# Performance work log

Measured on AMD Instinct MI355X. Metric: run time of the kernel, lower is better.

The kernel has to match this reference:

```python
import jax, jax.numpy as jnp
import numpy as np
import math

B, C, H, W = 32, 256, 64, 64
AUX, RANK, HID, OS = 64, 64, 256, 8


def _fourier(u):
    # u: [B, r] -> take first r//2, sin/cos with freqs linspace(1, pi)
    half = RANK // 2
    w = jnp.linspace(1.0, math.pi, half, dtype=u.dtype)[None, :]
    u = u[:, :half]
    return jnp.concatenate([jnp.sin(u * w), jnp.cos(u * w)], axis=-1)


def setup_inputs() -> dict:
    key = jax.random.key(0)
    ks = jax.random.split(key, 10)

    def lin(k, fan_in, fan_out):
        k1, k2 = jax.random.split(k)
        Wm = jax.random.normal(k1, (fan_in, fan_out), jnp.float32) * 0.02
        bv = jax.random.normal(k2, (fan_out,), jnp.float32) * 0.02
        return Wm, bv

    d = C + AUX
    W_pre, b_pre = lin(ks[0], d, HID)
    W_bc, b_bc = lin(ks[1], HID, C)
    W_bs, b_bs = lin(ks[2], HID, OS)
    W_pc, b_pc = lin(ks[3], HID, RANK)
    W_ps, b_ps = lin(ks[4], HID, RANK)
    W_Wc, b_Wc = lin(ks[5], HID, C * RANK)
    W_Ws, b_Ws = lin(ks[6], HID, OS * RANK)
    x = jax.random.normal(ks[7], (B, C, H, W), jnp.float32)
    a = jax.random.normal(ks[8], (B, AUX), jnp.float32)
    return dict(x=x, a=a, W_pre=W_pre, b_pre=b_pre, W_bc=W_bc, b_bc=b_bc,
                W_bs=W_bs, b_bs=b_bs, W_pc=W_pc, b_pc=b_pc, W_ps=W_ps,
                b_ps=b_ps, W_Wc=W_Wc, b_Wc=b_Wc, W_Ws=W_Ws, b_Ws=b_Ws)


def _m2dm(x, a, W_pre, b_pre, W_bc, b_bc, W_bs, b_bs, W_pc, b_pc,
          W_ps, b_ps, W_Wc, b_Wc, W_Ws, b_Ws):
    Bn, Cn, Hn, Wn = x.shape
    # DynamicProjection
    g = x.mean(axis=(2, 3))                                    # [B,C] GAP
    h = jax.nn.relu(jnp.concatenate([g, a], axis=-1) @ W_pre + b_pre)
    m_base_c = h @ W_bc + b_bc                                 # [B,C]
    m_base_s = h @ W_bs + b_bs                                 # [B,8]
    phi_c = _fourier(h @ W_pc + b_pc)                          # [B,r]
    phi_s = _fourier(h @ W_ps + b_ps)                          # [B,r]
    Wc = (h @ W_Wc + b_Wc).reshape(Bn, Cn, RANK)
    Ws = (h @ W_Ws + b_Ws).reshape(Bn, OS, RANK)
    c_m = m_base_c * jnp.einsum('bcr,br->bc', Wc, phi_c)
    s_m = m_base_s * jnp.einsum('bsr,br->bs', Ws, phi_s)

    # channel modulation
    xc = x * jax.nn.sigmoid(c_m)[:, :, None, None]

    # SpatialModulation: per-sample cross-shaped 3x3 stencil on [avg,max]
    av = x.mean(axis=1)
    mx = x.max(axis=1)
    y = jnp.stack([av, mx], axis=1)                            # [B,2,H,W]
    p = s_m[:, :8].reshape(Bn, 2, 4)                           # up,down,left,right

    def shift(z, di, dj):
        # s[h,w] = z[h+di, w+dj] with zero padding (matches conv2d padding=1)
        zp = jnp.pad(z, ((0, 0), (0, 0), (1, 1), (1, 1)))
        return zp[:, :, 1 + di:1 + di + Hn, 1 + dj:1 + dj + Wn]

    up = shift(y, -1, 0)   # k[0,1] pairs with input row h-1
    dn = shift(y, 1, 0)    # k[2,1]
    lf = shift(y, 0, -1)   # k[1,0]
    rt = shift(y, 0, 1)    # k[1,2]
    pw = p[..., None, None]                                    # [B,2,4,1,1]
    center = -p.sum(axis=-1)[..., None, None]                  # k[1,1] = -sum
    conv = (pw[:, :, 0] * up + pw[:, :, 1] * dn +
            pw[:, :, 2] * lf + pw[:, :, 3] * rt + center * y).sum(axis=1)  # [B,H,W]
    xs = x * jax.nn.sigmoid(conv)[:, None, :, :]
    return x + xc + xs


def reference(x, a, W_pre, b_pre, W_bc, b_bc, W_bs, b_bs, W_pc, b_pc,
              W_ps, b_ps, W_Wc, b_Wc, W_Ws, b_Ws):
    return _m2dm(x, a, W_pre, b_pre, W_bc, b_bc, W_bs, b_bs, W_pc, b_pc,
                 W_ps, b_ps, W_Wc, b_Wc, W_Ws, b_Ws)
```

## Files before the change

### kernel.cpp

```cpp
#include <hip/hip_runtime.h>
#include <math.h>

#define BN   32
#define CN   256
#define HWN  4096
#define AUXN 64
#define RANKN 64
#define HIDN 256
#define OSN  8

#define WS_GPART 0
#define WS_HT    131072
#define WS_PHIC  139264
#define WS_MBC   141312
#define WS_SM    149504
#define WS_SIGC  149760
#define WS_Y     157952
#define WS_SIGS  420096

__global__ __launch_bounds__(256) void k_stats(const float* __restrict__ x,
                                               float* __restrict__ gpart,
                                               float* __restrict__ y) {
  int b = blockIdx.y, tile = blockIdx.x, t = threadIdx.x;
  int w = t >> 6, l = t & 63;
  __shared__ float csum[256 * 65];
  __shared__ float4 s_comb[4][64];
  __shared__ float4 m_comb[4][64];
  const float4* xb4 = (const float4*)(x + (size_t)b * CN * HWN + tile * 256);
  float4 s4 = {0.f, 0.f, 0.f, 0.f};
  float4 m4 = {-INFINITY, -INFINITY, -INFINITY, -INFINITY};
  int c0 = w << 6;
#pragma unroll 8
  for (int cl = 0; cl < 64; cl++) {
    int c = c0 + cl;
    float4 v = xb4[(size_t)c * 1024 + l];
    s4.x += v.x; s4.y += v.y; s4.z += v.z; s4.w += v.w;
    m4.x = fmaxf(m4.x, v.x); m4.y = fmaxf(m4.y, v.y);
    m4.z = fmaxf(m4.z, v.z); m4.w = fmaxf(m4.w, v.w);
    csum[c * 65 + l] = (v.x + v.y) + (v.z + v.w);
  }
  s_comb[w][l] = s4;
  m_comb[w][l] = m4;
  __syncthreads();
  {
    const volatile float* row = csum + t * 65;
    float g0 = 0.f, g1 = 0.f, g2 = 0.f, g3 = 0.f;
#pragma unroll
    for (int j = 0; j < 64; j += 4) {
      g0 += row[j]; g1 += row[j + 1]; g2 += row[j + 2]; g3 += row[j + 3];
    }
    gpart[(((size_t)b * 16 + tile) << 8) + t] = (g0 + g1) + (g2 + g3);
  }
  if (w == 0) {
    float4 a0 = s_comb[0][l], a1 = s_comb[1][l], a2 = s_comb[2][l], a3 = s_comb[3][l];
    float4 b0 = m_comb[0][l], b1 = m_comb[1][l], b2 = m_comb[2][l], b3 = m_comb[3][l];
    float4 sa, ma;
    sa.x = (a0.x + a1.x) + (a2.x + a3.x);
    sa.y = (a0.y + a1.y) + (a2.y + a3.y);
    sa.z = (a0.z + a1.z) + (a2.z + a3.z);
    sa.w = (a0.w + a1.w) + (a2.w + a3.w);
    ma.x = fmaxf(fmaxf(b0.x, b1.x), fmaxf(b2.x, b3.x));
    ma.y = fmaxf(fmaxf(b0.y, b1.y), fmaxf(b2.y, b3.y));
    ma.z = fmaxf(fmaxf(b0.z, b1.z), fmaxf(b2.z, b3.z));
    ma.w = fmaxf(fmaxf(b0.w, b1.w), fmaxf(b2.w, b3.w));
    const float inv = 1.0f / 256.0f;
    float4 avg = {sa.x * inv, sa.y * inv, sa.z * inv, sa.w * inv};
    ((float4*)(y + (size_t)b * 2 * HWN + tile * 256))[l] = avg;
    ((float4*)(y + ((size_t)b * 2 + 1) * HWN + tile * 256))[l] = ma;
  }
}

__global__ __launch_bounds__(256) void k_head(
    const float* __restrict__ gpart, const float* __restrict__ a,
    const float* __restrict__ W_pre, const float* __restrict__ b_pre,
    const float* __restrict__ W_bc,  const float* __restrict__ b_bc,
    const float* __restrict__ W_bs,  const float* __restrict__ b_bs,
    const float* __restrict__ W_pc,  const float* __restrict__ b_pc,
    const float* __restrict__ W_ps,  const float* __restrict__ b_ps,
    const float* __restrict__ W_Ws,  const float* __restrict__ b_Ws,
    const float* __restrict__ y,
    float* __restrict__ h_t_out, float* __restrict__ phic_out,
    float* __restrict__ mbc_out, float* __restrict__ sigs) {
  int b = blockIdx.x, t = threadIdx.x;
  __shared__ float in_s[320];
  __shared__ float h_s[256];
  __shared__ float phic_s[64], phis_s[64];
  __shared__ float red[512];
  __shared__ float red2[256];
  __shared__ float pc[10];
  {
    float gsum = 0.f;
#pragma unroll
    for (int tile = 0; tile < 16; tile++)
      gsum += gpart[(((size_t)b * 16 + tile) << 8) + t];
    in_s[t] = gsum * (1.0f / 4096.0f);
  }
  if (t < 64) in_s[256 + t] = a[b * 64 + t];
  __syncthreads();
  float acc = b_pre[t];
  for (int k = 0; k < 320; k++) acc = fmaf(in_s[k], W_pre[k * 256 + t], acc);
  float h = fmaxf(acc, 0.f);
  h_s[t] = h;
  h_t_out[t * 32 + b] = h;
  __syncthreads();
  {
    int ui = t & 63, kg = t >> 6, j = ui & 31;
    const float* Wp = (ui < 32) ? W_pc : W_ps;
    float u = 0.f;
    int k0 = kg << 6;
    for (int k = k0; k < k0 + 64; k++) u = fmaf(h_s[k], Wp[k * 64 + j], u);
    red2[(ui << 2) | kg] = u;
  }
  __syncthreads();
  if (t < 64) {
    int j = t & 31;
    const float* bp = (t < 32) ? b_pc : b_ps;
    float u = bp[j] + (red2[t * 4] + red2[t * 4 + 1]) + (red2[t * 4 + 2] + red2[t * 4 + 3]);
    float wj = 1.0f + (float)j * (3.14159265358979323846f - 1.0f) / 31.0f;
    float su = sinf(u * wj), cu = cosf(u * wj);
    float* ph = (t < 32) ? phic_s : phis_s;
    ph[j] = su;
    ph[32 + j] = cu;
  }
  __syncthreads();
  if (t < 64) phic_out[b * 64 + t] = phic_s[t];
  float mb = b_bc[t];
  for (int k = 0; k < 256; k++) mb = fmaf(h_s[k], W_bc[k * 256 + t], mb);
  mbc_out[b * 256 + t] = mb;
#pragma unroll
  for (int i = 0; i < 2; i++) {
    int idx = t + 256 * i;
    int s = idx >> 6, r = idx & 63;
    float v = b_Ws[s * 64 + r];
    for (int k = 0; k < 256; k++) v = fmaf(h_s[k], W_Ws[k * 512 + s * 64 + r], v);
    red[idx] = v * phis_s[r];
  }
  {
    int s = t & 7, kg = t >> 3;
    float v = 0.f;
    int k0 = kg << 3;
#pragma unroll
    for (int k = k0; k < k0 + 8; k++) v = fmaf(h_s[k], W_bs[k * 8 + s], v);
    red2[t] = v;
  }
  __syncthreads();
  if (t < 8) {
    float mbs = b_bs[t];
#pragma unroll
    for (int kg = 0; kg < 32; kg++) mbs += red2[kg * 8 + t];
    float sum = 0.f;
    for (int r = 0; r < 64; r++) sum += red[t * 64 + r];
    pc[t] = mbs * sum;
  }
  __syncthreads();
  if (t == 0) {
    pc[8] = -(pc[0] + pc[1] + pc[2] + pc[3]);
    pc[9] = -(pc[4] + pc[5] + pc[6] + pc[7]);
  }
  __syncthreads();
  const float* yb = y + (size_t)b * 2 * HWN;
  for (int px = t; px < 4096; px += 256) {
    int i = px >> 6, j = px & 63;
    float conv = 0.f;
#pragma unroll
    for (int k = 0; k < 2; k++) {
      const float* yk = yb + k * 4096;
      float up = (i > 0)  ? yk[px - 64] : 0.f;
      float dn = (i < 63) ? yk[px + 64] : 0.f;
      float lf = (j > 0)  ? yk[px - 1]  : 0.f;
      float rt = (j < 63) ? yk[px + 1]  : 0.f;
      conv += pc[k * 4 + 0] * up + pc[k * 4 + 1] * dn + pc[k * 4 + 2] * lf +
              pc[k * 4 + 3] * rt + pc[8 + k] * yk[px];
    }
    sigs[b * 4096 + px] = 1.f / (1.f + expf(-conv));
  }
}

__global__ __launch_bounds__(512) void k_cm(
    const float* __restrict__ W_Wc, const float* __restrict__ b_Wc,
    const float* __restrict__ h_t, const float* __restrict__ phic_ws,
    const float* __restrict__ mbc_ws, float* __restrict__ sigc_out) {
  __shared__ __align__(16) float wsl[16384];
  __shared__ __align__(16) float h_s[8192];
  __shared__ __align__(16) float phi_s[2048];
  __shared__ float red[4096];
  __shared__ float red2[512];
  int t = threadIdx.x, c = blockIdx.x;
  {
    const float4* col4 = (const float4*)(W_Wc + (size_t)c * 64);
    float4* wsl4 = (float4*)wsl;
#pragma unroll
    for (int i4 = t; i4 < 4096; i4 += 512) {
      int k = i4 >> 4, rq = i4 & 15;
      wsl4[i4] = col4[(size_t)k * 4096 + rq];
    }
    const float4* ht4 = (const float4*)h_t;
    float4* hs4 = (float4*)h_s;
#pragma unroll
    for (int i4 = t; i4 < 2048; i4 += 512) hs4[i4] = ht4[i4];
    ((float4*)phi_s)[t] = ((const float4*)phic_ws)[t];
  }
  __syncthreads();
  int rq = t & 15, b8 = (t >> 4) & 3, kg = t >> 6;
  const float4* wv = (const float4*)wsl;
  float4 acc[8];
#pragma unroll
  for (int i = 0; i < 8; i++) acc[i] = {0.f, 0.f, 0.f, 0.f};
#pragma unroll 4
  for (int kk = 0; kk < 32; kk++) {
    int k = (kg << 5) + kk;
    float4 w4 = wv[k * 16 + rq];
    const float4* hp = (const float4*)(h_s + k * 32 + (b8 << 3));
    float4 h0 = hp[0], h1 = hp[1];
    float hv[8] = {h0.x, h0.y, h0.z, h0.w, h1.x, h1.y, h1.z, h1.w};
#pragma unroll
    for (int i = 0; i < 8; i++) {
      acc[i].x = fmaf(hv[i], w4.x, acc[i].x);
      acc[i].y = fmaf(hv[i], w4.y, acc[i].y);
      acc[i].z = fmaf(hv[i], w4.z, acc[i].z);
      acc[i].w = fmaf(hv[i], w4.w, acc[i].w);
    }
  }
  float4 bw = {0.f, 0.f, 0.f, 0.f};
  if (kg == 0) bw = ((const float4*)(b_Wc + (size_t)c * 64))[rq];
#pragma unroll
  for (int i = 0; i < 8; i++) {
    int bb = (b8 << 3) + i;
    float4 ph = ((const float4*)phi_s)[bb * 16 + rq];
    float4 av = acc[i];
    av.x += bw.x; av.y += bw.y; av.z += bw.z; av.w += bw.w;
    red[(kg * 32 + bb) * 16 + rq] =
        (av.x * ph.x + av.y * ph.y) + (av.z * ph.z + av.w * ph.w);
  }
  __syncthreads();
  {
    int bb = t >> 4, rr = t & 15;
    float tot = 0.f;
#pragma unroll
    for (int g = 0; g < 8; g++) tot += red[(g * 32 + bb) * 16 + rr];
    red2[t] = tot;
  }
  __syncthreads();
  if (t < 32) {
    float sum = 0.f;
#pragma unroll
    for (int i = 0; i < 16; i++) sum += red2[t * 16 + i];
    float v = mbc_ws[t * 256 + c] * sum;
    sigc_out[t * 256 + c] = 1.f / (1.f + expf(-v));
  }
}

__global__ __launch_bounds__(256) void k_final(const float* __restrict__ x,
                                               const float* __restrict__ sigc,
                                               const float* __restrict__ sigs,
                                               float* __restrict__ out) {
  size_t idx4 = (size_t)blockIdx.x * 256 + threadIdx.x;
  size_t flat = idx4 * 4;
  int b = (int)(flat >> 20);
  int c = (int)((flat >> 12) & 255);
  int px = (int)(flat & 4095);
  float4 xv = ((const float4*)x)[idx4];
  float sc = 1.0f + sigc[b * 256 + c];
  float4 ss = ((const float4*)sigs)[((size_t)b * HWN + px) >> 2];
  float4 o;
  o.x = xv.x * (sc + ss.x);
  o.y = xv.y * (sc + ss.y);
  o.z = xv.z * (sc + ss.z);
  o.w = xv.w * (sc + ss.w);
  ((float4*)out)[idx4] = o;
}

extern "C" void kernel_launch(void* const* d_in, const int* in_sizes, int n_in,
                              void* d_out, int out_size, void* d_ws, size_t ws_size,
                              hipStream_t stream) {
  const float* x     = (const float*)d_in[0];
  const float* a     = (const float*)d_in[1];
  const float* W_pre = (const float*)d_in[2];
  const float* b_pre = (const float*)d_in[3];
  const float* W_bc  = (const float*)d_in[4];
  const float* b_bc  = (const float*)d_in[5];
  const float* W_bs  = (const float*)d_in[6];
  const float* b_bs  = (const float*)d_in[7];
  const float* W_pc  = (const float*)d_in[8];
  const float* b_pc  = (const float*)d_in[9];
  const float* W_ps  = (const float*)d_in[10];
  const float* b_ps  = (const float*)d_in[11];
  const float* W_Wc  = (const float*)d_in[12];
  const float* b_Wc  = (const float*)d_in[13];
  const float* W_Ws  = (const float*)d_in[14];
  const float* b_Ws  = (const float*)d_in[15];
  float* out = (float*)d_out;
  float* ws  = (float*)d_ws;

  float* gpart_ws = ws + WS_GPART;
  float* ht_ws    = ws + WS_HT;
  float* phic_ws  = ws + WS_PHIC;
  float* mbc_ws   = ws + WS_MBC;
  float* sigc_ws  = ws + WS_SIGC;
  float* y_ws     = ws + WS_Y;
  float* sigs_ws  = ws + WS_SIGS;

  k_stats<<<dim3(16, BN), 256, 0, stream>>>(x, gpart_ws, y_ws);
  k_head<<<BN, 256, 0, stream>>>(gpart_ws, a, W_pre, b_pre, W_bc, b_bc, W_bs, b_bs,
                                 W_pc, b_pc, W_ps, b_ps, W_Ws, b_Ws, y_ws,
                                 ht_ws, phic_ws, mbc_ws, sigs_ws);
  k_cm<<<CN, 512, 0, stream>>>(W_Wc, b_Wc, ht_ws, phic_ws, mbc_ws, sigc_ws);
  k_final<<<(BN * CN * HWN) / 4 / 256, 256, 0, stream>>>(x, sigc_ws, sigs_ws, out);
}
```

Before: 343.3 us.

## Fuse all stages into one persistent kernel with grid-wide atomic barriers

Replaces the four kernel launches with a single persistent kernel of 256 blocks that uses atomic-counter grid barriers between the stats, head, channel-modulation and final stages. The W_Wc slice load is issued before the head-stage barrier so it overlaps the per-sample head work, and the m_base_c projection moves into the channel stage. The final elementwise pass becomes a grid-stride loop over 256 blocks instead of a large launch. This removes launch gaps and inter-kernel drains, but the streaming stages now run on only 256 blocks at a fixed occupancy and rely on all blocks being co-resident for the spin barriers.

```diff
diff --git a/kernel.cpp b/kernel.cpp
--- a/kernel.cpp
+++ b/kernel.cpp
@@ -4,270 +4,315 @@
 #define BN   32
 #define CN   256
 #define HWN  4096
-#define AUXN 64
-#define RANKN 64
-#define HIDN 256
-#define OSN  8
 
 #define WS_GPART 0
 #define WS_HT    131072
 #define WS_PHIC  139264
-#define WS_MBC   141312
-#define WS_SM    149504
+#define WS_BAR   149504
 #define WS_SIGC  149760
 #define WS_Y     157952
 #define WS_SIGS  420096
 
-__global__ __launch_bounds__(256) void k_stats(const float* __restrict__ x,
-                                               float* __restrict__ gpart,
-                                               float* __restrict__ y) {
-  int b = blockIdx.y, tile = blockIdx.x, t = threadIdx.x;
-  int w = t >> 6, l = t & 63;
-  __shared__ float csum[256 * 65];
-  __shared__ float4 s_comb[4][64];
-  __shared__ float4 m_comb[4][64];
-  const float4* xb4 = (const float4*)(x + (size_t)b * CN * HWN + tile * 256);
-  float4 s4 = {0.f, 0.f, 0.f, 0.f};
-  float4 m4 = {-INFINITY, -INFINITY, -INFINITY, -INFINITY};
-  int c0 = w << 6;
-#pragma unroll 8
-  for (int cl = 0; cl < 64; cl++) {
-    int c = c0 + cl;
-    float4 v = xb4[(size_t)c * 1024 + l];
-    s4.x += v.x; s4.y += v.y; s4.z += v.z; s4.w += v.w;
-    m4.x = fmaxf(m4.x, v.x); m4.y = fmaxf(m4.y, v.y);
-    m4.z = fmaxf(m4.z, v.z); m4.w = fmaxf(m4.w, v.w);
-    csum[c * 65 + l] = (v.x + v.y) + (v.z + v.w);
-  }
-  s_comb[w][l] = s4;
-  m_comb[w][l] = m4;
+
+__global__ __launch_bounds__(64) void k_init(float* __restrict__ ws) {
+  if (threadIdx.x < 3) ((unsigned*)(ws + WS_BAR))[threadIdx.x] = 0u;
+}
+
+__device__ __forceinline__ void grid_bar(unsigned* ctr) {
   __syncthreads();
-  {
-    const volatile float* row = csum + t * 65;
-    float g0 = 0.f, g1 = 0.f, g2 = 0.f, g3 = 0.f;
-#pragma unroll
-    for (int j = 0; j < 64; j += 4) {
-      g0 += row[j]; g1 += row[j + 1]; g2 += row[j + 2]; g3 += row[j + 3];
-    }
-    gpart[(((size_t)b * 16 + tile) << 8) + t] = (g0 + g1) + (g2 + g3);
-  }
-  if (w == 0) {
-    float4 a0 = s_comb[0][l], a1 = s_comb[1][l], a2 = s_comb[2][l], a3 = s_comb[3][l];
-    float4 b0 = m_comb[0][l], b1 = m_comb[1][l], b2 = m_comb[2][l], b3 = m_comb[3][l];
-    float4 sa, ma;
-    sa.x = (a0.x + a1.x) + (a2.x + a3.x);
-    sa.y = (a0.y + a1.y) + (a2.y + a3.y);
-    sa.z = (a0.z + a1.z) + (a2.z + a3.z);
-    sa.w = (a0.w + a1.w) + (a2.w + a3.w);
-    ma.x = fmaxf(fmaxf(b0.x, b1.x), fmaxf(b2.x, b3.x));
-    ma.y = fmaxf(fmaxf(b0.y, b1.y), fmaxf(b2.y, b3.y));
-    ma.z = fmaxf(fmaxf(b0.z, b1.z), fmaxf(b2.z, b3.z));
-    ma.w = fmaxf(fmaxf(b0.w, b1.w), fmaxf(b2.w, b3.w));
-    const float inv = 1.0f / 256.0f;
-    float4 avg = {sa.x * inv, sa.y * inv, sa.z * inv, sa.w * inv};
-    ((float4*)(y + (size_t)b * 2 * HWN + tile * 256))[l] = avg;
-    ((float4*)(y + ((size_t)b * 2 + 1) * HWN + tile * 256))[l] = ma;
-  }
+  if (threadIdx.x == 0) {
+    __threadfence();
+    atomicAdd(ctr, 1u);
+    while (__hip_atomic_load(ctr, __ATOMIC_ACQUIRE, __HIP_MEMORY_SCOPE_AGENT) < 256u) {
+      __builtin_amdgcn_s_sleep(2);
+    }
+  }
+  __syncthreads();
 }
 
-__global__ __launch_bounds__(256) void k_head(
-    const float* __restrict__ gpart, const float* __restrict__ a,
+__global__ __launch_bounds__(512, 2) void k_fused(
+    const float* __restrict__ x,     const float* __restrict__ a,
     const float* __restrict__ W_pre, const float* __restrict__ b_pre,
     const float* __restrict__ W_bc,  const float* __restrict__ b_bc,
     const float* __restrict__ W_bs,  const float* __restrict__ b_bs,
     const float* __restrict__ W_pc,  const float* __restrict__ b_pc,
     const float* __restrict__ W_ps,  const float* __restrict__ b_ps,
+    const float* __restrict__ W_Wc,  const float* __restrict__ b_Wc,
     const float* __restrict__ W_Ws,  const float* __restrict__ b_Ws,
-    const float* __restrict__ y,
-    float* __restrict__ h_t_out, float* __restrict__ phic_out,
-    float* __restrict__ mbc_out, float* __restrict__ sigs) {
-  int b = blockIdx.x, t = threadIdx.x;
-  __shared__ float in_s[320];
-  __shared__ float h_s[256];
-  __shared__ float phic_s[64], phis_s[64];
-  __shared__ float red[512];
-  __shared__ float red2[256];
-  __shared__ float pc[10];
+    float* __restrict__ out, float* __restrict__ ws) {
+  __shared__ __align__(16) float smem[31744];
+  const int t = threadIdx.x, blk = blockIdx.x;
+  float* gpart   = ws + WS_GPART;
+  float* ht      = ws + WS_HT;
+  float* phic    = ws + WS_PHIC;
+  unsigned* bar  = (unsigned*)(ws + WS_BAR);
+  float* sigc    = ws + WS_SIGC;
+  float* yws     = ws + WS_Y;
+  float* sigs    = ws + WS_SIGS;
+
   {
-    float gsum = 0.f;
-#pragma unroll
-    for (int tile = 0; tile < 16; tile++)
-      gsum += gpart[(((size_t)b * 16 + tile) << 8) + t];
-    in_s[t] = gsum * (1.0f / 4096.0f);
-  }
-  if (t < 64) in_s[256 + t] = a[b * 64 + t];
-  __syncthreads();
-  float acc = b_pre[t];
-  for (int k = 0; k < 320; k++) acc = fmaf(in_s[k], W_pre[k * 256 + t], acc);
-  float h = fmaxf(acc, 0.f);
-  h_s[t] = h;
-  h_t_out[t * 32 + b] = h;
-  __syncthreads();
+    int b = blk >> 3;
+    int w = t >> 6, l = t & 63;
+    const float4* xb = (const float4*)(x + (size_t)b * CN * HWN);
+    for (int rep = 0; rep < 2; ++rep) {
+      int tile = ((blk & 7) << 1) + rep;
+      const float4* xt = xb + tile * 64;
+      float4 s4 = {0.f, 0.f, 0.f, 0.f};
+      float4 m4 = {-INFINITY, -INFINITY, -INFINITY, -INFINITY};
+      int c0 = w << 5;
+#pragma unroll 8
+      for (int cl = 0; cl < 32; ++cl) {
+        int c = c0 + cl;
+        float4 v = xt[(size_t)c * 1024 + l];
+        s4.x += v.x; s4.y += v.y; s4.z += v.z; s4.w += v.w;
+        m4.x = fmaxf(m4.x, v.x); m4.y = fmaxf(m4.y, v.y);
+        m4.z = fmaxf(m4.z, v.z); m4.w = fmaxf(m4.w, v.w);
+        smem[c * 65 + l] = (v.x + v.y) + (v.z + v.w);
+      }
+      ((float4*)(smem + 16640))[(w << 6) + l] = s4;
+      ((float4*)(smem + 18688))[(w << 6) + l] = m4;
+      __syncthreads();
+      if (t < 256) {
+        const volatile float* row = smem + t * 65;
+        float g0 = 0.f, g1 = 0.f, g2 = 0.f, g3 = 0.f;
+#pragma unroll
+        for (int j = 0; j < 64; j += 4) {
+          g0 += row[j]; g1 += row[j + 1]; g2 += row[j + 2]; g3 += row[j + 3];
+        }
+        gpart[(((size_t)b * 16 + tile) << 8) + t] = (g0 + g1) + (g2 + g3);
+      } else if (t < 320) {
+        int l2 = t - 256;
+        const float4* sc4 = (const float4*)(smem + 16640);
+        const float4* mc4 = (const float4*)(smem + 18688);
+        float4 sa = sc4[l2], ma = mc4[l2];
+#pragma unroll
+        for (int w2 = 1; w2 < 8; ++w2) {
+          float4 s2 = sc4[(w2 << 6) + l2], m2 = mc4[(w2 << 6) + l2];
+          sa.x += s2.x; sa.y += s2.y; sa.z += s2.z; sa.w += s2.w;
+          ma.x = fmaxf(ma.x, m2.x); ma.y = fmaxf(ma.y, m2.y);
+          ma.z = fmaxf(ma.z, m2.z); ma.w = fmaxf(ma.w, m2.w);
+        }
+        const float inv = 1.0f / 256.0f;
+        float4 av = {sa.x * inv, sa.y * inv, sa.z * inv, sa.w * inv};
+        ((float4*)(yws + (size_t)b * 2 * HWN + tile * 256))[l2] = av;
+        ((float4*)(yws + ((size_t)b * 2 + 1) * HWN + tile * 256))[l2] = ma;
+      }
+      __syncthreads();
+    }
+  }
+  grid_bar(bar + 0);
+
   {
-    int ui = t & 63, kg = t >> 6, j = ui & 31;
-    const float* Wp = (ui < 32) ? W_pc : W_ps;
-    float u = 0.f;
-    int k0 = kg << 6;
-    for (int k = k0; k < k0 + 64; k++) u = fmaf(h_s[k], Wp[k * 64 + j], u);
-    red2[(ui << 2) | kg] = u;
-  }
-  __syncthreads();
-  if (t < 64) {
-    int j = t & 31;
-    const float* bp = (t < 32) ? b_pc : b_ps;
-    float u = bp[j] + (red2[t * 4] + red2[t * 4 + 1]) + (red2[t * 4 + 2] + red2[t * 4 + 3]);
-    float wj = 1.0f + (float)j * (3.14159265358979323846f - 1.0f) / 31.0f;
-    float su = sinf(u * wj), cu = cosf(u * wj);
-    float* ph = (t < 32) ? phic_s : phis_s;
-    ph[j] = su;
-    ph[32 + j] = cu;
-  }
-  __syncthreads();
-  if (t < 64) phic_out[b * 64 + t] = phic_s[t];
-  float mb = b_bc[t];
-  for (int k = 0; k < 256; k++) mb = fmaf(h_s[k], W_bc[k * 256 + t], mb);
-  mbc_out[b * 256 + t] = mb;
-#pragma unroll
-  for (int i = 0; i < 2; i++) {
-    int idx = t + 256 * i;
-    int s = idx >> 6, r = idx & 63;
-    float v = b_Ws[s * 64 + r];
-    for (int k = 0; k < 256; k++) v = fmaf(h_s[k], W_Ws[k * 512 + s * 64 + r], v);
-    red[idx] = v * phis_s[r];
-  }
-  {
-    int s = t & 7, kg = t >> 3;
-    float v = 0.f;
-    int k0 = kg << 3;
-#pragma unroll
-    for (int k = k0; k < k0 + 8; k++) v = fmaf(h_s[k], W_bs[k * 8 + s], v);
-    red2[t] = v;
-  }
-  __syncthreads();
-  if (t < 8) {
-    float mbs = b_bs[t];
-#pragma unroll
-    for (int kg = 0; kg < 32; kg++) mbs += red2[kg * 8 + t];
-    float sum = 0.f;
-    for (int r = 0; r < 64; r++) sum += red[t * 64 + r];
-    pc[t] = mbs * sum;
-  }
-  __syncthreads();
-  if (t == 0) {
-    pc[8] = -(pc[0] + pc[1] + pc[2] + pc[3]);
-    pc[9] = -(pc[4] + pc[5] + pc[6] + pc[7]);
-  }
-  __syncthreads();
-  const float* yb = y + (size_t)b * 2 * HWN;
-  for (int px = t; px < 4096; px += 256) {
-    int i = px >> 6, j = px & 63;
-    float conv = 0.f;
-#pragma unroll
-    for (int k = 0; k < 2; k++) {
-      const float* yk = yb + k * 4096;
-      float up = (i > 0)  ? yk[px - 64] : 0.f;
-      float dn = (i < 63) ? yk[px + 64] : 0.f;
-      float lf = (j > 0)  ? yk[px - 1]  : 0.f;
-      float rt = (j < 63) ? yk[px + 1]  : 0.f;
-      conv += pc[k * 4 + 0] * up + pc[k * 4 + 1] * dn + pc[k * 4 + 2] * lf +
-              pc[k * 4 + 3] * rt + pc[8 + k] * yk[px];
-    }
-    sigs[b * 4096 + px] = 1.f / (1.f + expf(-conv));
-  }
-}
-
-__global__ __launch_bounds__(512) void k_cm(
-    const float* __restrict__ W_Wc, const float* __restrict__ b_Wc,
-    const float* __restrict__ h_t, const float* __restrict__ phic_ws,
-    const float* __restrict__ mbc_ws, float* __restrict__ sigc_out) {
-  __shared__ __align__(16) float wsl[16384];
-  __shared__ __align__(16) float h_s[8192];
-  __shared__ __align__(16) float phi_s[2048];
-  __shared__ float red[4096];
-  __shared__ float red2[512];
-  int t = threadIdx.x, c = blockIdx.x;
-  {
-    const float4* col4 = (const float4*)(W_Wc + (size_t)c * 64);
-    float4* wsl4 = (float4*)wsl;
-#pragma unroll
-    for (int i4 = t; i4 < 4096; i4 += 512) {
+    const float4* col4 = (const float4*)(W_Wc + (size_t)blk * 64);
+    float4* wsl4 = (float4*)smem;
+#pragma unroll
+    for (int j = 0; j < 8; ++j) {
+      int i4 = t + (j << 9);
       int k = i4 >> 4, rq = i4 & 15;
       wsl4[i4] = col4[(size_t)k * 4096 + rq];
     }
-    const float4* ht4 = (const float4*)h_t;
-    float4* hs4 = (float4*)h_s;
-#pragma unroll
-    for (int i4 = t; i4 < 2048; i4 += 512) hs4[i4] = ht4[i4];
-    ((float4*)phi_s)[t] = ((const float4*)phic_ws)[t];
-  }
-  __syncthreads();
-  int rq = t & 15, b8 = (t >> 4) & 3, kg = t >> 6;
-  const float4* wv = (const float4*)wsl;
-  float4 acc[8];
-#pragma unroll
-  for (int i = 0; i < 8; i++) acc[i] = {0.f, 0.f, 0.f, 0.f};
+    if (blk < 32) {
+      int b = blk;
+      float* in_s  = smem + 26624;
+      float* hs    = smem + 26944;
+      float* phis  = smem + 27200;
+      float* hred  = smem + 27264;
+      float* hred2 = smem + 27776;
+      float* mbsr  = smem + 28288;
+      float* pcb   = smem + 28800;
+      if (t < 256) {
+        float g = 0.f;
+#pragma unroll
+        for (int tl = 0; tl < 16; ++tl) g += gpart[(((size_t)b * 16 + tl) << 8) + t];
+        in_s[t] = g * (1.0f / 4096.0f);
+      } else if (t < 320) {
+        in_s[t] = a[(b << 6) + t - 256];
+      }
+      __syncthreads();
+      {
+        int o = t & 255, half = t >> 8;
+        float acc = half ? 0.f : b_pre[o];
+        int k0 = half * 160;
+        for (int k = k0; k < k0 + 160; ++k) acc = fmaf(in_s[k], W_pre[(k << 8) + o], acc);
+        hred[(half << 8) + o] = acc;
+      }
+      __syncthreads();
+      if (t < 256) {
+        float h = fmaxf(hred[t] + hred[256 + t], 0.f);
+        hs[t] = h;
+        ht[(t << 5) + b] = h;
+      }
+      __syncthreads();
+      {
+        int ui = t & 63, kg = t >> 6, j = ui & 31;
+        const float* Wp = (ui < 32) ? W_pc : W_ps;
+        float u = 0.f;
+        int k0 = kg << 5;
+#pragma unroll 8
+        for (int k = k0; k < k0 + 32; ++k) u = fmaf(hs[k], Wp[(k << 6) + j], u);
+        hred2[(ui << 3) + kg] = u;
+      }
+      __syncthreads();
+      if (t < 64) {
+        int j = t & 31;
+        const float* bp = (t < 32) ? b_pc : b_ps;
+        float u = bp[j];
+#pragma unroll
+        for (int g = 0; g < 8; ++g) u += hred2[(t << 3) + g];
+        float wj = 1.0f + (float)j * ((3.14159265358979323846f - 1.0f) / 31.0f);
+        float su = sinf(u * wj), cu = cosf(u * wj);
+        if (t < 32) { phic[(b << 6) + j] = su; phic[(b << 6) + 32 + j] = cu; }
+        else        { phis[j] = su; phis[32 + j] = cu; }
+      }
+      __syncthreads();
+      {
+        int r = t & 63;
+        float v = b_Ws[t];
+        for (int k = 0; k < 256; ++k) v = fmaf(hs[k], W_Ws[(k << 9) + t], v);
+        hred[t] = v * phis[r];
+        int sg = t & 7, kq = t >> 3;
+        float mv = 0.f;
+        int k0 = kq << 2;
+#pragma unroll
+        for (int k = k0; k < k0 + 4; ++k) mv = fmaf(hs[k], W_bs[(k << 3) + sg], mv);
+        mbsr[t] = mv;
+      }
+      __syncthreads();
+      if (t < 8) {
+        float mbs = b_bs[t];
+#pragma unroll
+        for (int g = 0; g < 64; ++g) mbs += mbsr[(g << 3) + t];
+        float sum = 0.f;
+#pragma unroll
+        for (int r = 0; r < 64; ++r) sum += hred[(t << 6) + r];
+        pcb[t] = mbs * sum;
+      }
+      __syncthreads();
+      if (t == 0) {
+        pcb[8] = -(pcb[0] + pcb[1] + pcb[2] + pcb[3]);
+        pcb[9] = -(pcb[4] + pcb[5] + pcb[6] + pcb[7]);
+      }
+      __syncthreads();
+      const float* yb = yws + (size_t)b * 2 * HWN;
+#pragma unroll
+      for (int rep = 0; rep < 8; ++rep) {
+        int px = t + (rep << 9);
+        int i = px >> 6, j = px & 63;
+        float conv = 0.f;
+#pragma unroll
+        for (int k = 0; k < 2; ++k) {
+          const float* yk = yb + (k << 12);
+          float up = (i > 0)  ? yk[px - 64] : 0.f;
+          float dn = (i < 63) ? yk[px + 64] : 0.f;
+          float lf = (j > 0)  ? yk[px - 1]  : 0.f;
+          float rt = (j < 63) ? yk[px + 1]  : 0.f;
+          conv += pcb[(k << 2) + 0] * up + pcb[(k << 2) + 1] * dn +
+                  pcb[(k << 2) + 2] * lf + pcb[(k << 2) + 3] * rt + pcb[8 + k] * yk[px];
+        }
+        sigs[(b << 12) + px] = 1.f / (1.f + expf(-conv));
+      }
+    }
+  }
+  grid_bar(bar + 1);
+
+  {
+    int c = blk;
+    float* h3   = smem + 16384;
+    float* phi3 = smem + 24576;
+    float* red  = smem + 26624;
+    float* red2 = smem + 30720;
+    float* mred = smem + 31232;
+    {
+      const float4* ht4 = (const float4*)ht;
+      float4* h34 = (float4*)h3;
+#pragma unroll
+      for (int j = 0; j < 4; ++j) h34[t + (j << 9)] = ht4[t + (j << 9)];
+      ((float4*)phi3)[t] = ((const float4*)phic)[t];
+    }
+    __syncthreads();
+    int rq = t & 15, b8 = (t >> 4) & 3, kg = t >> 6;
+    const float4* wv = (const float4*)smem;
+    float4 acc[8];
+#pragma unroll
+    for (int i = 0; i < 8; ++i) acc[i] = {0.f, 0.f, 0.f, 0.f};
 #pragma unroll 4
-  for (int kk = 0; kk < 32; kk++) {
-    int k = (kg << 5) + kk;
-    float4 w4 = wv[k * 16 + rq];
-    const float4* hp = (const float4*)(h_s + k * 32 + (b8 << 3));
-    float4 h0 = hp[0], h1 = hp[1];
-    float hv[8] = {h0.x, h0.y, h0.z, h0.w, h1.x, h1.y, h1.z, h1.w};
-#pragma unroll
-    for (int i = 0; i < 8; i++) {
-      acc[i].x = fmaf(hv[i], w4.x, acc[i].x);
-      acc[i].y = fmaf(hv[i], w4.y, acc[i].y);
-      acc[i].z = fmaf(hv[i], w4.z, acc[i].z);
-      acc[i].w = fmaf(hv[i], w4.w, acc[i].w);
-    }
-  }
-  float4 bw = {0.f, 0.f, 0.f, 0.f};
-  if (kg == 0) bw = ((const float4*)(b_Wc + (size_t)c * 64))[rq];
-#pragma unroll
-  for (int i = 0; i < 8; i++) {
-    int bb = (b8 << 3) + i;
-    float4 ph = ((const float4*)phi_s)[bb * 16 + rq];
-    float4 av = acc[i];
-    av.x += bw.x; av.y += bw.y; av.z += bw.z; av.w += bw.w;
-    red[(kg * 32 + bb) * 16 + rq] =
-        (av.x * ph.x + av.y * ph.y) + (av.z * ph.z + av.w * ph.w);
-  }
-  __syncthreads();
+    for (int kk = 0; kk < 32; ++kk) {
+      int k = (kg << 5) + kk;
+      float4 w4 = wv[(k << 4) + rq];
+      const float4* hp = (const float4*)(h3 + (k << 5) + (b8 << 3));
+      float4 h0 = hp[0], h1 = hp[1];
+      float hv[8] = {h0.x, h0.y, h0.z, h0.w, h1.x, h1.y, h1.z, h1.w};
+#pragma unroll
+      for (int i = 0; i < 8; ++i) {
+        acc[i].x = fmaf(hv[i], w4.x, acc[i].x);
+        acc[i].y = fmaf(hv[i], w4.y, acc[i].y);
+        acc[i].z = fmaf(hv[i], w4.z, acc[i].z);
+        acc[i].w = fmaf(hv[i], w4.w, acc[i].w);
+      }
+    }
+    {
+      int bb = t & 31, kq = t >> 5;
+      float mv = 0.f;
+      int k0 = kq << 4;
+#pragma unroll
+      for (int k = k0; k < k0 + 16; ++k) mv = fmaf(h3[(k << 5) + bb], W_bc[(k << 8) + c], mv);
+      mred[t] = mv;
+    }
+    float4 bw = {0.f, 0.f, 0.f, 0.f};
+    if (kg == 0) bw = ((const float4*)(b_Wc + (size_t)c * 64))[rq];
+#pragma unroll
+    for (int i = 0; i < 8; ++i) {
+      int bb = (b8 << 3) + i;
+      float4 ph = ((const float4*)phi3)[(bb << 4) + rq];
+      float4 av = acc[i];
+      av.x += bw.x; av.y += bw.y; av.z += bw.z; av.w += bw.w;
+      red[((kg << 5) + bb) * 16 + rq] =
+          (av.x * ph.x + av.y * ph.y) + (av.z * ph.z + av.w * ph.w);
+    }
+    __syncthreads();
+    {
+      int bb = t >> 4, rr = t & 15;
+      float tot = 0.f;
+#pragma unroll
+      for (int g = 0; g < 8; ++g) tot += red[((g << 5) + bb) * 16 + rr];
+      red2[t] = tot;
+    }
+    __syncthreads();
+    if (t < 32) {
+      float sum = 0.f;
+#pragma unroll
+      for (int i = 0; i < 16; ++i) sum += red2[(t << 4) + i];
+      float mb = b_bc[c];
+#pragma unroll
+      for (int g = 0; g < 16; ++g) mb += mred[(g << 5) + t];
+      float v = mb * sum;
+      sigc[(t << 8) + c] = 1.f / (1.f + expf(-v));
+    }
+  }
+  grid_bar(bar + 2);
+
   {
-    int bb = t >> 4, rr = t & 15;
-    float tot = 0.f;
-#pragma unroll
-    for (int g = 0; g < 8; g++) tot += red[(g * 32 + bb) * 16 + rr];
-    red2[t] = tot;
-  }
-  __syncthreads();
-  if (t < 32) {
-    float sum = 0.f;
-#pragma unroll
-    for (int i = 0; i < 16; i++) sum += red2[t * 16 + i];
-    float v = mbc_ws[t * 256 + c] * sum;
-    sigc_out[t * 256 + c] = 1.f / (1.f + expf(-v));
-  }
-}
-
-__global__ __launch_bounds__(256) void k_final(const float* __restrict__ x,
-                                               const float* __restrict__ sigc,
-                                               const float* __restrict__ sigs,
-                                               float* __restrict__ out) {
-  size_t idx4 = (size_t)blockIdx.x * 256 + threadIdx.x;
-  size_t flat = idx4 * 4;
-  int b = (int)(flat >> 20);
-  int c = (int)((flat >> 12) & 255);
-  int px = (int)(flat & 4095);
-  float4 xv = ((const float4*)x)[idx4];
-  float sc = 1.0f + sigc[b * 256 + c];
-  float4 ss = ((const float4*)sigs)[((size_t)b * HWN + px) >> 2];
-  float4 o;
-  o.x = xv.x * (sc + ss.x);
-  o.y = xv.y * (sc + ss.y);
-  o.z = xv.z * (sc + ss.z);
-  o.w = xv.w * (sc + ss.w);
-  ((float4*)out)[idx4] = o;
+    const float4* x4 = (const float4*)x;
+    const float4* s4v = (const float4*)sigs;
+    float4* o4 = (float4*)out;
+    size_t base = ((size_t)blk << 9) + t;
+#pragma unroll 4
+    for (int it = 0; it < 64; ++it) {
+      size_t idx4 = base + ((size_t)it << 17);
+      size_t flat = idx4 << 2;
+      int b = (int)(flat >> 20);
+      int cc = (int)((flat >> 12) & 255);
+      float4 xv = x4[idx4];
+      float sc = 1.0f + sigc[(b << 8) + cc];
+      float4 ss = s4v[((size_t)b << 10) + (idx4 & 1023)];
+      float4 o;
+      o.x = xv.x * (sc + ss.x);
+      o.y = xv.y * (sc + ss.y);
+      o.z = xv.z * (sc + ss.z);
+      o.w = xv.w * (sc + ss.w);
+      o4[idx4] = o;
+    }
+  }
 }
 
 extern "C" void kernel_launch(void* const* d_in, const int* in_sizes, int n_in,
@@ -292,18 +337,8 @@
   float* out = (float*)d_out;
   float* ws  = (float*)d_ws;
 
-  float* gpart_ws = ws + WS_GPART;
-  float* ht_ws    = ws + WS_HT;
-  float* phic_ws  = ws + WS_PHIC;
-  float* mbc_ws   = ws + WS_MBC;
-  float* sigc_ws  = ws + WS_SIGC;
-  float* y_ws     = ws + WS_Y;
-  float* sigs_ws  = ws + WS_SIGS;
-
-  k_stats<<<dim3(16, BN), 256, 0, stream>>>(x, gpart_ws, y_ws);
-  k_head<<<BN, 256, 0, stream>>>(gpart_ws, a, W_pre, b_pre, W_bc, b_bc, W_bs, b_bs,
-                                 W_pc, b_pc, W_ps, b_ps, W_Ws, b_Ws, y_ws,
-                                 ht_ws, phic_ws, mbc_ws, sigs_ws);
-  k_cm<<<CN, 512, 0, stream>>>(W_Wc, b_Wc, ht_ws, phic_ws, mbc_ws, sigc_ws);
-  k_final<<<(BN * CN * HWN) / 4 / 256, 256, 0, stream>>>(x, sigc_ws, sigs_ws, out);
+  k_init<<<1, 64, 0, stream>>>(ws);
+  k_fused<<<256, 512, 0, stream>>>(x, a, W_pre, b_pre, W_bc, b_bc, W_bs, b_bs,
+                                   W_pc, b_pc, W_ps, b_ps, W_Wc, b_Wc, W_Ws, b_Ws,
+                                   out, ws);
 }
```

Result: slower. 430.4 us (+25.4%).

## Halve k_stats shared memory and widen k_head to 512 threads

Applied to the files above, without the earlier changes.

k_stats now processes channels in two halves, so its per-channel partial-sum buffer in shared memory is half the size, and it declares launch bounds with a minimum of 3 blocks per SM. This raises occupancy for the memory-bound statistics pass at the cost of extra barriers. k_head doubles its thread count and splits the serial K-loops of the small matvecs (W_pre, W_bc, W_pc/W_ps, W_Ws, W_bs) across more threads, reducing per-block latency for this 32-block kernel. Index arithmetic elsewhere is cosmetically rewritten with shifts.

```diff
diff --git a/kernel.cpp b/kernel.cpp
--- a/kernel.cpp
+++ b/kernel.cpp
@@ -4,73 +4,71 @@
 #define BN   32
 #define CN   256
 #define HWN  4096
-#define AUXN 64
-#define RANKN 64
-#define HIDN 256
-#define OSN  8
 
 #define WS_GPART 0
 #define WS_HT    131072
 #define WS_PHIC  139264
 #define WS_MBC   141312
-#define WS_SM    149504
 #define WS_SIGC  149760
 #define WS_Y     157952
 #define WS_SIGS  420096
 
-__global__ __launch_bounds__(256) void k_stats(const float* __restrict__ x,
-                                               float* __restrict__ gpart,
-                                               float* __restrict__ y) {
+__global__ __launch_bounds__(256, 3) void k_stats(const float* __restrict__ x,
+                                                  float* __restrict__ gpart,
+                                                  float* __restrict__ y) {
   int b = blockIdx.y, tile = blockIdx.x, t = threadIdx.x;
   int w = t >> 6, l = t & 63;
-  __shared__ float csum[256 * 65];
-  __shared__ float4 s_comb[4][64];
-  __shared__ float4 m_comb[4][64];
-  const float4* xb4 = (const float4*)(x + (size_t)b * CN * HWN + tile * 256);
+  __shared__ float csum[128 * 65];
+  __shared__ float4 s_comb[256];
+  __shared__ float4 m_comb[256];
+  const float4* xt = (const float4*)(x + (size_t)b * CN * HWN) + tile * 64;
   float4 s4 = {0.f, 0.f, 0.f, 0.f};
   float4 m4 = {-INFINITY, -INFINITY, -INFINITY, -INFINITY};
-  int c0 = w << 6;
+  float* gp = gpart + (((size_t)b * 16 + tile) << 8);
+  for (int cc = 0; cc < 2; ++cc) {
+    int cbase = cc << 7;
 #pragma unroll 8
-  for (int cl = 0; cl < 64; cl++) {
-    int c = c0 + cl;
-    float4 v = xb4[(size_t)c * 1024 + l];
-    s4.x += v.x; s4.y += v.y; s4.z += v.z; s4.w += v.w;
-    m4.x = fmaxf(m4.x, v.x); m4.y = fmaxf(m4.y, v.y);
-    m4.z = fmaxf(m4.z, v.z); m4.w = fmaxf(m4.w, v.w);
-    csum[c * 65 + l] = (v.x + v.y) + (v.z + v.w);
-  }
-  s_comb[w][l] = s4;
-  m_comb[w][l] = m4;
-  __syncthreads();
-  {
-    const volatile float* row = csum + t * 65;
-    float g0 = 0.f, g1 = 0.f, g2 = 0.f, g3 = 0.f;
-#pragma unroll
-    for (int j = 0; j < 64; j += 4) {
-      g0 += row[j]; g1 += row[j + 1]; g2 += row[j + 2]; g3 += row[j + 3];
-    }
-    gpart[(((size_t)b * 16 + tile) << 8) + t] = (g0 + g1) + (g2 + g3);
-  }
+    for (int cl = 0; cl < 32; ++cl) {
+      int cp = (w << 5) + cl;
+      int c = cbase + cp;
+      float4 v = xt[(size_t)c * 1024 + l];
+      s4.x += v.x; s4.y += v.y; s4.z += v.z; s4.w += v.w;
+      m4.x = fmaxf(m4.x, v.x); m4.y = fmaxf(m4.y, v.y);
+      m4.z = fmaxf(m4.z, v.z); m4.w = fmaxf(m4.w, v.w);
+      csum[cp * 65 + l] = (v.x + v.y) + (v.z + v.w);
+    }
+    __syncthreads();
+    if (t < 128) {
+      const volatile float* row = csum + t * 65;
+      float g0 = 0.f, g1 = 0.f, g2 = 0.f, g3 = 0.f;
+#pragma unroll
+      for (int j = 0; j < 64; j += 4) {
+        g0 += row[j]; g1 += row[j + 1]; g2 += row[j + 2]; g3 += row[j + 3];
+      }
+      gp[cbase + t] = (g0 + g1) + (g2 + g3);
+    }
+    __syncthreads();
+  }
+  s_comb[(w << 6) + l] = s4;
+  m_comb[(w << 6) + l] = m4;
+  __syncthreads();
   if (w == 0) {
-    float4 a0 = s_comb[0][l], a1 = s_comb[1][l], a2 = s_comb[2][l], a3 = s_comb[3][l];
-    float4 b0 = m_comb[0][l], b1 = m_comb[1][l], b2 = m_comb[2][l], b3 = m_comb[3][l];
-    float4 sa, ma;
-    sa.x = (a0.x + a1.x) + (a2.x + a3.x);
-    sa.y = (a0.y + a1.y) + (a2.y + a3.y);
-    sa.z = (a0.z + a1.z) + (a2.z + a3.z);
-    sa.w = (a0.w + a1.w) + (a2.w + a3.w);
-    ma.x = fmaxf(fmaxf(b0.x, b1.x), fmaxf(b2.x, b3.x));
-    ma.y = fmaxf(fmaxf(b0.y, b1.y), fmaxf(b2.y, b3.y));
-    ma.z = fmaxf(fmaxf(b0.z, b1.z), fmaxf(b2.z, b3.z));
-    ma.w = fmaxf(fmaxf(b0.w, b1.w), fmaxf(b2.w, b3.w));
+    float4 sa = s_comb[l], ma = m_comb[l];
+#pragma unroll
+    for (int w2 = 1; w2 < 4; ++w2) {
+      float4 s2 = s_comb[(w2 << 6) + l], m2 = m_comb[(w2 << 6) + l];
+      sa.x += s2.x; sa.y += s2.y; sa.z += s2.z; sa.w += s2.w;
+      ma.x = fmaxf(ma.x, m2.x); ma.y = fmaxf(ma.y, m2.y);
+      ma.z = fmaxf(ma.z, m2.z); ma.w = fmaxf(ma.w, m2.w);
+    }
     const float inv = 1.0f / 256.0f;
-    float4 avg = {sa.x * inv, sa.y * inv, sa.z * inv, sa.w * inv};
-    ((float4*)(y + (size_t)b * 2 * HWN + tile * 256))[l] = avg;
+    float4 av = {sa.x * inv, sa.y * inv, sa.z * inv, sa.w * inv};
+    ((float4*)(y + (size_t)b * 2 * HWN + tile * 256))[l] = av;
     ((float4*)(y + ((size_t)b * 2 + 1) * HWN + tile * 256))[l] = ma;
   }
 }
 
-__global__ __launch_bounds__(256) void k_head(
+__global__ __launch_bounds__(512) void k_head(
     const float* __restrict__ gpart, const float* __restrict__ a,
     const float* __restrict__ W_pre, const float* __restrict__ b_pre,
     const float* __restrict__ W_bc,  const float* __restrict__ b_bc,
@@ -79,100 +77,112 @@
     const float* __restrict__ W_ps,  const float* __restrict__ b_ps,
     const float* __restrict__ W_Ws,  const float* __restrict__ b_Ws,
     const float* __restrict__ y,
-    float* __restrict__ h_t_out, float* __restrict__ phic_out,
+    float* __restrict__ ht, float* __restrict__ phic,
     float* __restrict__ mbc_out, float* __restrict__ sigs) {
   int b = blockIdx.x, t = threadIdx.x;
-  __shared__ float in_s[320];
-  __shared__ float h_s[256];
-  __shared__ float phic_s[64], phis_s[64];
-  __shared__ float red[512];
-  __shared__ float red2[256];
-  __shared__ float pc[10];
-  {
-    float gsum = 0.f;
-#pragma unroll
-    for (int tile = 0; tile < 16; tile++)
-      gsum += gpart[(((size_t)b * 16 + tile) << 8) + t];
-    in_s[t] = gsum * (1.0f / 4096.0f);
-  }
-  if (t < 64) in_s[256 + t] = a[b * 64 + t];
-  __syncthreads();
-  float acc = b_pre[t];
-  for (int k = 0; k < 320; k++) acc = fmaf(in_s[k], W_pre[k * 256 + t], acc);
-  float h = fmaxf(acc, 0.f);
-  h_s[t] = h;
-  h_t_out[t * 32 + b] = h;
+  __shared__ float in_s[320], hs[256], phis[64];
+  __shared__ float sA[512], sB[512], sC[512], sD[512];
+  __shared__ float pcb[16];
+  if (t < 256) {
+    float g = 0.f;
+#pragma unroll
+    for (int tl = 0; tl < 16; ++tl) g += gpart[(((size_t)b * 16 + tl) << 8) + t];
+    in_s[t] = g * (1.0f / 4096.0f);
+  } else if (t < 320) {
+    in_s[t] = a[(b << 6) + t - 256];
+  }
+  __syncthreads();
+  {
+    int o = t & 255, half = t >> 8;
+    float acc = half ? 0.f : b_pre[o];
+    int k0 = half * 160;
+    for (int k = k0; k < k0 + 160; ++k) acc = fmaf(in_s[k], W_pre[(k << 8) + o], acc);
+    sA[(half << 8) + o] = acc;
+  }
+  __syncthreads();
+  if (t < 256) {
+    float h = fmaxf(sA[t] + sA[256 + t], 0.f);
+    hs[t] = h;
+    ht[(t << 5) + b] = h;
+  }
   __syncthreads();
   {
     int ui = t & 63, kg = t >> 6, j = ui & 31;
     const float* Wp = (ui < 32) ? W_pc : W_ps;
     float u = 0.f;
-    int k0 = kg << 6;
-    for (int k = k0; k < k0 + 64; k++) u = fmaf(h_s[k], Wp[k * 64 + j], u);
-    red2[(ui << 2) | kg] = u;
+    int k0 = kg << 5;
+#pragma unroll 8
+    for (int k = k0; k < k0 + 32; ++k) u = fmaf(hs[k], Wp[(k << 6) + j], u);
+    sB[(ui << 3) + kg] = u;
+  }
+  {
+    int o = t & 255, half = t >> 8;
+    float mb = half ? 0.f : b_bc[o];
+    int k0 = half << 7;
+    for (int k = k0; k < k0 + 128; ++k) mb = fmaf(hs[k], W_bc[(k << 8) + o], mb);
+    sC[(half << 8) + o] = mb;
   }
   __syncthreads();
   if (t < 64) {
     int j = t & 31;
     const float* bp = (t < 32) ? b_pc : b_ps;
-    float u = bp[j] + (red2[t * 4] + red2[t * 4 + 1]) + (red2[t * 4 + 2] + red2[t * 4 + 3]);
-    float wj = 1.0f + (float)j * (3.14159265358979323846f - 1.0f) / 31.0f;
+    float u = bp[j];
+#pragma unroll
+    for (int g = 0; g < 8; ++g) u += sB[(t << 3) + g];
+    float wj = 1.0f + (float)j * ((3.14159265358979323846f - 1.0f) / 31.0f);
     float su = sinf(u * wj), cu = cosf(u * wj);
-    float* ph = (t < 32) ? phic_s : phis_s;
-    ph[j] = su;
-    ph[32 + j] = cu;
-  }
-  __syncthreads();
-  if (t < 64) phic_out[b * 64 + t] = phic_s[t];
-  float mb = b_bc[t];
-  for (int k = 0; k < 256; k++) mb = fmaf(h_s[k], W_bc[k * 256 + t], mb);
-  mbc_out[b * 256 + t] = mb;
-#pragma unroll
-  for (int i = 0; i < 2; i++) {
-    int idx = t + 256 * i;
-    int s = idx >> 6, r = idx & 63;
-    float v = b_Ws[s * 64 + r];
-    for (int k = 0; k < 256; k++) v = fmaf(h_s[k], W_Ws[k * 512 + s * 64 + r], v);
-    red[idx] = v * phis_s[r];
-  }
-  {
-    int s = t & 7, kg = t >> 3;
-    float v = 0.f;
-    int k0 = kg << 3;
-#pragma unroll
-    for (int k = k0; k < k0 + 8; k++) v = fmaf(h_s[k], W_bs[k * 8 + s], v);
-    red2[t] = v;
+    if (t < 32) { phic[(b << 6) + j] = su; phic[(b << 6) + 32 + j] = cu; }
+    else        { phis[j] = su; phis[32 + j] = cu; }
+  } else if (t >= 256) {
+    int o = t - 256;
+    mbc_out[(b << 8) + o] = sC[o] + sC[256 + o];
+  }
+  __syncthreads();
+  {
+    int r = t & 63;
+    float v = b_Ws[t];
+    for (int k = 0; k < 256; ++k) v = fmaf(hs[k], W_Ws[(k << 9) + t], v);
+    sD[t] = v * phis[r];
+    int sg = t & 7, kq = t >> 3;
+    float mv = 0.f;
+    int k0 = kq << 2;
+#pragma unroll
+    for (int k = k0; k < k0 + 4; ++k) mv = fmaf(hs[k], W_bs[(k << 3) + sg], mv);
+    sA[t] = mv;
   }
   __syncthreads();
   if (t < 8) {
     float mbs = b_bs[t];
 #pragma unroll
-    for (int kg = 0; kg < 32; kg++) mbs += red2[kg * 8 + t];
+    for (int g = 0; g < 64; ++g) mbs += sA[(g << 3) + t];
     float sum = 0.f;
-    for (int r = 0; r < 64; r++) sum += red[t * 64 + r];
-    pc[t] = mbs * sum;
+#pragma unroll
+    for (int r = 0; r < 64; ++r) sum += sD[(t << 6) + r];
+    pcb[t] = mbs * sum;
   }
   __syncthreads();
   if (t == 0) {
-    pc[8] = -(pc[0] + pc[1] + pc[2] + pc[3]);
-    pc[9] = -(pc[4] + pc[5] + pc[6] + pc[7]);
+    pcb[8] = -(pcb[0] + pcb[1] + pcb[2] + pcb[3]);
+    pcb[9] = -(pcb[4] + pcb[5] + pcb[6] + pcb[7]);
   }
   __syncthreads();
   const float* yb = y + (size_t)b * 2 * HWN;
-  for (int px = t; px < 4096; px += 256) {
+#pragma unroll
+  for (int rep = 0; rep < 8; ++rep) {
+    int px = t + (rep << 9);
     int i = px >> 6, j = px & 63;
     float conv = 0.f;
 #pragma unroll
-    for (int k = 0; k < 2; k++) {
-      const float* yk = yb + k * 4096;
+    for (int k = 0; k < 2; ++k) {
+      const float* yk = yb + (k << 12);
       float up = (i > 0)  ? yk[px - 64] : 0.f;
       float dn = (i < 63) ? yk[px + 64] : 0.f;
       float lf = (j > 0)  ? yk[px - 1]  : 0.f;
       float rt = (j < 63) ? yk[px + 1]  : 0.f;
-      conv += pc[k * 4 + 0] * up + pc[k * 4 + 1] * dn + pc[k * 4 + 2] * lf +
-              pc[k * 4 + 3] * rt + pc[8 + k] * yk[px];
-    }
-    sigs[b * 4096 + px] = 1.f / (1.f + expf(-conv));
+      conv += pcb[(k << 2) + 0] * up + pcb[(k << 2) + 1] * dn +
+              pcb[(k << 2) + 2] * lf + pcb[(k << 2) + 3] * rt + pcb[8 + k] * yk[px];
+    }
+    sigs[(b << 12) + px] = 1.f / (1.f + expf(-conv));
   }
 }
 
@@ -205,16 +215,16 @@
   const float4* wv = (const float4*)wsl;
   float4 acc[8];
 #pragma unroll
-  for (int i = 0; i < 8; i++) acc[i] = {0.f, 0.f, 0.f, 0.f};
+  for (int i = 0; i < 8; ++i) acc[i] = {0.f, 0.f, 0.f, 0.f};
 #pragma unroll 4
-  for (int kk = 0; kk < 32; kk++) {
+  for (int kk = 0; kk < 32; ++kk) {
     int k = (kg << 5) + kk;
-    float4 w4 = wv[k * 16 + rq];
-    const float4* hp = (const float4*)(h_s + k * 32 + (b8 << 3));
+    float4 w4 = wv[(k << 4) + rq];
+    const float4* hp = (const float4*)(h_s + (k << 5) + (b8 << 3));
     float4 h0 = hp[0], h1 = hp[1];
     float hv[8] = {h0.x, h0.y, h0.z, h0.w, h1.x, h1.y, h1.z, h1.w};
 #pragma unroll
-    for (int i = 0; i < 8; i++) {
+    for (int i = 0; i < 8; ++i) {
       acc[i].x = fmaf(hv[i], w4.x, acc[i].x);
       acc[i].y = fmaf(hv[i], w4.y, acc[i].y);
       acc[i].z = fmaf(hv[i], w4.z, acc[i].z);
@@ -224,12 +234,12 @@
   float4 bw = {0.f, 0.f, 0.f, 0.f};
   if (kg == 0) bw = ((const float4*)(b_Wc + (size_t)c * 64))[rq];
 #pragma unroll
-  for (int i = 0; i < 8; i++) {
+  for (int i = 0; i < 8; ++i) {
     int bb = (b8 << 3) + i;
-    float4 ph = ((const float4*)phi_s)[bb * 16 + rq];
+    float4 ph = ((const float4*)phi_s)[(bb << 4) + rq];
     float4 av = acc[i];
     av.x += bw.x; av.y += bw.y; av.z += bw.z; av.w += bw.w;
-    red[(kg * 32 + bb) * 16 + rq] =
+    red[((kg << 5) + bb) * 16 + rq] =
         (av.x * ph.x + av.y * ph.y) + (av.z * ph.z + av.w * ph.w);
   }
   __syncthreads();
@@ -237,16 +247,16 @@
     int bb = t >> 4, rr = t & 15;
     float tot = 0.f;
 #pragma unroll
-    for (int g = 0; g < 8; g++) tot += red[(g * 32 + bb) * 16 + rr];
+    for (int g = 0; g < 8; ++g) tot += red[((g << 5) + bb) * 16 + rr];
     red2[t] = tot;
   }
   __syncthreads();
   if (t < 32) {
     float sum = 0.f;
 #pragma unroll
-    for (int i = 0; i < 16; i++) sum += red2[t * 16 + i];
-    float v = mbc_ws[t * 256 + c] * sum;
-    sigc_out[t * 256 + c] = 1.f / (1.f + expf(-v));
+    for (int i = 0; i < 16; ++i) sum += red2[(t << 4) + i];
+    float v = mbc_ws[(t << 8) + c] * sum;
+    sigc_out[(t << 8) + c] = 1.f / (1.f + expf(-v));
   }
 }
 
@@ -301,7 +311,7 @@
   float* sigs_ws  = ws + WS_SIGS;
 
   k_stats<<<dim3(16, BN), 256, 0, stream>>>(x, gpart_ws, y_ws);
-  k_head<<<BN, 256, 0, stream>>>(gpart_ws, a, W_pre, b_pre, W_bc, b_bc, W_bs, b_bs,
+  k_head<<<BN, 512, 0, stream>>>(gpart_ws, a, W_pre, b_pre, W_bc, b_bc, W_bs, b_bs,
                                  W_pc, b_pc, W_ps, b_ps, W_Ws, b_Ws, y_ws,
                                  ht_ws, phic_ws, mbc_ws, sigs_ws);
   k_cm<<<CN, 512, 0, stream>>>(W_Wc, b_Wc, ht_ws, phic_ws, mbc_ws, sigc_ws);
```

New measurement: 345.6 us. About the same (+0.7%).
